# Optimization experiments

Hardware: AMD Instinct MI355X
Metric: run time of the kernel (lower is better)

## Reference

```python
import jax, jax.numpy as jnp
import numpy as np
from jax import lax

WIN = 5
WIN_SIZE = float(WIN * WIN * WIN)


def _box_sum(x):
    # 5x5x5 all-ones box-filter sum, stride 1, padding 2 (SAME), single channel.
    k = jnp.ones((1, 1, WIN, WIN, WIN), dtype=x.dtype)
    return lax.conv_general_dilated(
        x, k,
        window_strides=(1, 1, 1),
        padding=[(2, 2), (2, 2), (2, 2)],
        dimension_numbers=('NCDHW', 'OIDHW', 'NCDHW'))


def setup_inputs() -> dict:
    key = jax.random.key(0)
    k1, k2 = jax.random.split(key)
    shape = (2, 1, 160, 160, 160)
    real = jax.random.normal(k1, shape, dtype=jnp.float32)
    fake = jax.random.normal(k2, shape, dtype=jnp.float32)
    return {"real": real, "fake": fake}


def reference(real, fake):
    I2 = real * real
    J2 = fake * fake
    IJ = real * fake
    I_sum = _box_sum(real)
    J_sum = _box_sum(fake)
    I2_sum = _box_sum(I2)
    J2_sum = _box_sum(J2)
    IJ_sum = _box_sum(IJ)
    u_I = I_sum / WIN_SIZE
    u_J = J_sum / WIN_SIZE
    cross = IJ_sum - u_J * I_sum - u_I * J_sum + u_I * u_J * WIN_SIZE
    I_var = I2_sum - 2.0 * u_I * I_sum + u_I * u_I * WIN_SIZE
    J_var = J2_sum - 2.0 * u_J * J_sum + u_J * u_J * WIN_SIZE
    cc = cross * cross / (I_var * J_var + 1e-05)
    return jnp.mean(cc)
```

## Files before the change

kernel.cpp:

```cpp
#include <hip/hip_runtime.h>


#define DIM 160
#define SLAB (DIM * DIM)
#define VOL (DIM * DIM * DIM)
#define TD 8
#define ROWS 36
#define RST 44
#define NBLK 1000
#define NPART (NBLK * 4)

typedef float f4 __attribute__((ext_vector_type(4), aligned(16)));
typedef float f2 __attribute__((ext_vector_type(2), aligned(8)));

__device__ __forceinline__ f4 hwin(const f4 lo, const f4 hi) {
    const float c0 = ((lo.x + lo.y) + (lo.z + lo.w)) + hi.x;
    const float c1 = c0 - lo.x + hi.y;
    const float c2 = c1 - lo.y + hi.z;
    const float c3 = c2 - lo.z + hi.w;
    return (f4){c0, c1, c2, c3};
}

__global__ __launch_bounds__(256, 2) void ncc_main(const float* __restrict__ real,
                                                   const float* __restrict__ fake,
                                                   float* __restrict__ partials) {
    __shared__ __align__(16) float raw[2][2][ROWS][RST];

    const int tid = threadIdx.x;

    const int bid = blockIdx.x;
    const int vid = (bid & 7) * 125 + (bid >> 3);
    const int dz  = vid % 20;
    const int t1  = vid / 20;
    const int bx  = t1 % 5;
    const int by  = (t1 / 5) % 5;
    const int nb  = t1 / 25;
    const int w0 = 32 * bx, h0 = 32 * by, d0 = TD * dz;

    const float* baseI = real + (size_t)nb * VOL;
    const float* baseJ = fake + (size_t)nb * VOL;

    const int sr = tid >> 3;
    const int sc = tid & 7;
    const int co = sr * RST + 4 * sc;

    int gof[3], lof[3];
    bool ok[3], wlo[3];
    const float* src[3];
#pragma unroll
    for (int k = 0; k < 3; ++k) {
        const int t   = tid + 256 * k;
        const int tv  = t / 360;
        const int rem = t - 360 * tv;
        const int row = rem / 10;
        const int q   = rem - 10 * row;
        const int hg  = h0 - 2 + row;
        const int wq  = w0 - 4 + 4 * q;
        const bool okh = (unsigned)hg < DIM;
        const bool okw = (wq >= 0) && (wq + 3 < DIM);
        ok[k]  = (t < 720) && okh && okw;
        wlo[k] = ok[k] && (q > 0);
        gof[k] = hg * DIM + wq;
        lof[k] = (tv * ROWS + row) * RST + 4 * q - 2;
        src[k] = tv ? baseJ : baseI;
    }

    {
        float* L = &raw[0][0][0][0];
        for (int i = tid; i < 2 * 2 * ROWS * RST; i += 256) L[i] = 0.f;
    }
    __syncthreads();

    if (d0 > 0) {
        const size_t so = (size_t)(d0 - 2) * SLAB;
        float* L = &raw[0][0][0][0];
#pragma unroll
        for (int k = 0; k < 3; ++k) {
            if (ok[k]) {
                const f4 v = *(const f4*)(src[k] + so + gof[k]);
                if (wlo[k]) *(f2*)(L + lof[k]) = (f2){v.x, v.y};
                *(f2*)(L + lof[k] + 2) = (f2){v.z, v.w};
            }
        }
    }
    __syncthreads();

    const f4 zf = (f4){0.f, 0.f, 0.f, 0.f};
    f4 zs[5][5];
#pragma unroll
    for (int p = 0; p < 5; ++p)
#pragma unroll
        for (int q = 0; q < 5; ++q) zs[p][q] = zf;

    f4 acc = zf;
    const float inv = 1.0f / 125.0f;
    int cur = 0;

#pragma unroll 1
    for (int a = 0; a < 3; ++a) {
        const bool am0 = (a > 0);
#pragma unroll
        for (int b = 0; b < 5; ++b) {
            const bool compAct  = (a < 2) || (b < 2);
            const bool stageAct = (a < 2) || (b == 0);
            if (!compAct) continue;

            f4 v0 = zf, v1 = zf, v2 = zf;
            if (stageAct) {
                const int dd1 = d0 - 1 + 5 * a + b;
                if ((unsigned)dd1 < DIM) {
                    const size_t so = (size_t)dd1 * SLAB;
                    if (ok[0]) v0 = *(const f4*)(src[0] + so + gof[0]);
                    if (ok[1]) v1 = *(const f4*)(src[1] + so + gof[1]);
                    if (ok[2]) v2 = *(const f4*)(src[2] + so + gof[2]);
                }
            }

            const float* LI = &raw[cur][0][0][0];
            const float* LJ = &raw[cur][1][0][0];
            f4 vI0 = zf, vI1 = zf, vJ0 = zf, vJ1 = zf;
            f4 vI20 = zf, vI21 = zf, vJ20 = zf, vJ21 = zf, vIJ0 = zf, vIJ1 = zf;
#pragma unroll
            for (int t = 0; t < 5; ++t) {
                const int o = co + t * RST;
                const f4 a0 = *(const f4*)(LI + o);
                const f4 a1 = *(const f4*)(LI + o + 4);
                const f4 b0 = *(const f4*)(LJ + o);
                const f4 b1 = *(const f4*)(LJ + o + 4);
                vI0 += a0; vI1 += a1; vJ0 += b0; vJ1 += b1;
                vI20 += a0 * a0; vI21 += a1 * a1;
                vJ20 += b0 * b0; vJ21 += b1 * b1;
                vIJ0 += a0 * b0; vIJ1 += a1 * b1;
            }
            const f4 cs0 = hwin(vI0, vI1);
            const f4 cs1 = hwin(vJ0, vJ1);
            const f4 cs2 = hwin(vI20, vI21);
            const f4 cs3 = hwin(vJ20, vJ21);
            const f4 cs4 = hwin(vIJ0, vIJ1);

#pragma unroll
            for (int p = 0; p < 5; ++p) {
                const int kk  = (b - p + 5) % 5;
                const int bmk = b - kk;
                const bool doadd = (am0 || p <= b) &&
                                   (a == 0 || (a == 1 ? (bmk <= 2) : (bmk <= -3)));
                if (doadd) {
                    zs[p][0] += cs0; zs[p][1] += cs1; zs[p][2] += cs2;
                    zs[p][3] += cs3; zs[p][4] += cs4;
                }
            }

            const bool docomp = (a == 0) ? (b == 4) : ((a == 1) ? true : (b < 2));
            if (docomp) {
                const int pe = (b + 1) % 5;
                const f4 SI = zs[pe][0], SJ = zs[pe][1];
                const f4 S2I = zs[pe][2], S2J = zs[pe][3], SIJ = zs[pe][4];
                const f4 t0    = SI * inv;
                const f4 cross = SIJ - t0 * SJ;
                const f4 iv    = S2I - t0 * SI;
                const f4 jv    = S2J - (SJ * inv) * SJ;
                acc += cross * cross / (iv * jv + 1e-5f);
                zs[pe][0] = zf; zs[pe][1] = zf; zs[pe][2] = zf;
                zs[pe][3] = zf; zs[pe][4] = zf;
            }

            if (stageAct) {
                float* L = &raw[cur ^ 1][0][0][0];
                if (wlo[0]) *(f2*)(L + lof[0]) = (f2){v0.x, v0.y};
                if (ok[0])  *(f2*)(L + lof[0] + 2) = (f2){v0.z, v0.w};
                if (wlo[1]) *(f2*)(L + lof[1]) = (f2){v1.x, v1.y};
                if (ok[1])  *(f2*)(L + lof[1] + 2) = (f2){v1.z, v1.w};
                if (wlo[2]) *(f2*)(L + lof[2]) = (f2){v2.x, v2.y};
                if (ok[2])  *(f2*)(L + lof[2] + 2) = (f2){v2.z, v2.w};
            }
            __syncthreads();
            cur ^= 1;
        }
    }

    float a2 = (acc.x + acc.y) + (acc.z + acc.w);
#pragma unroll
    for (int off = 32; off; off >>= 1)
        a2 += __shfl_down(a2, off, 64);
    if ((tid & 63) == 0)
        partials[bid * 4 + (tid >> 6)] = a2;
}

__global__ void ncc_reduce(const float* __restrict__ partials, float* __restrict__ out) {
    __shared__ double ws[4];
    double s = 0.0;
    for (int i = threadIdx.x; i < NPART; i += 256) s += (double)partials[i];
#pragma unroll
    for (int off = 32; off; off >>= 1)
        s += __shfl_down(s, off, 64);
    if ((threadIdx.x & 63) == 0) ws[threadIdx.x >> 6] = s;
    __syncthreads();
    if (threadIdx.x == 0) {
        const double t = ws[0] + ws[1] + ws[2] + ws[3];
        out[0] = (float)(t / (2.0 * (double)VOL));
    }
}

extern "C" void kernel_launch(void* const* d_in, const int* in_sizes, int n_in,
                              void* d_out, int out_size, void* d_ws, size_t ws_size,
                              hipStream_t stream) {
    const float* real = (const float*)d_in[0];
    const float* fake = (const float*)d_in[1];
    float* out      = (float*)d_out;
    float* partials = (float*)d_ws;

    ncc_main<<<dim3(NBLK), dim3(256), 0, stream>>>(real, fake, partials);
    ncc_reduce<<<1, 256, 0, stream>>>(partials, out);
}
```

Baseline: 53.28 us.

## Halve tile height to 16 rows, two outputs per thread, doubling block count

```diff
diff --git a/kernel.cpp b/kernel.cpp
--- a/kernel.cpp
+++ b/kernel.cpp
@@ -5,21 +5,14 @@
 #define SLAB (DIM * DIM)
 #define VOL (DIM * DIM * DIM)
 #define TD 8
-#define ROWS 36
+#define TH 16
+#define ROWS 20
 #define RST 44
-#define NBLK 1000
+#define NBLK 2000
 #define NPART (NBLK * 4)
 
 typedef float f4 __attribute__((ext_vector_type(4), aligned(16)));
 typedef float f2 __attribute__((ext_vector_type(2), aligned(8)));
-
-__device__ __forceinline__ f4 hwin(const f4 lo, const f4 hi) {
-    const float c0 = ((lo.x + lo.y) + (lo.z + lo.w)) + hi.x;
-    const float c1 = c0 - lo.x + hi.y;
-    const float c2 = c1 - lo.y + hi.z;
-    const float c3 = c2 - lo.z + hi.w;
-    return (f4){c0, c1, c2, c3};
-}
 
 __global__ __launch_bounds__(256, 2) void ncc_main(const float* __restrict__ real,
                                                    const float* __restrict__ fake,
@@ -29,45 +22,42 @@
     const int tid = threadIdx.x;
 
     const int bid = blockIdx.x;
-    const int vid = (bid & 7) * 125 + (bid >> 3);
+    const int vid = (bid & 7) * 250 + (bid >> 3);
     const int dz  = vid % 20;
     const int t1  = vid / 20;
     const int bx  = t1 % 5;
-    const int by  = (t1 / 5) % 5;
-    const int nb  = t1 / 25;
-    const int w0 = 32 * bx, h0 = 32 * by, d0 = TD * dz;
+    const int by  = (t1 / 5) % 10;
+    const int nb  = t1 / 50;
+    const int w0 = 32 * bx, h0 = TH * by, d0 = TD * dz;
 
     const float* baseI = real + (size_t)nb * VOL;
     const float* baseJ = fake + (size_t)nb * VOL;
 
-    const int sr = tid >> 3;
-    const int sc = tid & 7;
-    const int co = sr * RST + 4 * sc;
-
-    int gof[3], lof[3];
-    bool ok[3], wlo[3];
-    const float* src[3];
-#pragma unroll
-    for (int k = 0; k < 3; ++k) {
+    const int sc = tid & 15;
+    const int sr = tid >> 4;
+    const int co = sr * RST + 2 * sc + 2;
+
+    int gof[2], lof[2];
+    bool ok[2];
+    const float* src[2];
+#pragma unroll
+    for (int k = 0; k < 2; ++k) {
         const int t   = tid + 256 * k;
-        const int tv  = t / 360;
-        const int rem = t - 360 * tv;
+        const int vv  = t / 200;
+        const int rem = t - 200 * vv;
         const int row = rem / 10;
         const int q   = rem - 10 * row;
         const int hg  = h0 - 2 + row;
         const int wq  = w0 - 4 + 4 * q;
-        const bool okh = (unsigned)hg < DIM;
-        const bool okw = (wq >= 0) && (wq + 3 < DIM);
-        ok[k]  = (t < 720) && okh && okw;
-        wlo[k] = ok[k] && (q > 0);
+        ok[k]  = (t < 400) && ((unsigned)hg < DIM) && (wq >= 0) && (wq + 3 < DIM);
         gof[k] = hg * DIM + wq;
-        lof[k] = (tv * ROWS + row) * RST + 4 * q - 2;
-        src[k] = tv ? baseJ : baseI;
+        lof[k] = (vv * ROWS + row) * RST + 4 * q;
+        src[k] = vv ? baseJ : baseI;
     }
 
     {
         float* L = &raw[0][0][0][0];
-        for (int i = tid; i < 2 * 2 * ROWS * RST; i += 256) L[i] = 0.f;
+        for (int i = tid; i < 880; i += 256) *(f4*)(L + 4 * i) = (f4){0.f, 0.f, 0.f, 0.f};
     }
     __syncthreads();
 
@@ -75,24 +65,20 @@
         const size_t so = (size_t)(d0 - 2) * SLAB;
         float* L = &raw[0][0][0][0];
 #pragma unroll
-        for (int k = 0; k < 3; ++k) {
-            if (ok[k]) {
-                const f4 v = *(const f4*)(src[k] + so + gof[k]);
-                if (wlo[k]) *(f2*)(L + lof[k]) = (f2){v.x, v.y};
-                *(f2*)(L + lof[k] + 2) = (f2){v.z, v.w};
-            }
-        }
+        for (int k = 0; k < 2; ++k)
+            if (ok[k]) *(f4*)(L + lof[k]) = *(const f4*)(src[k] + so + gof[k]);
     }
     __syncthreads();
 
+    const f2 z2 = (f2){0.f, 0.f};
     const f4 zf = (f4){0.f, 0.f, 0.f, 0.f};
-    f4 zs[5][5];
+    f2 zs[5][5];
 #pragma unroll
     for (int p = 0; p < 5; ++p)
 #pragma unroll
-        for (int q = 0; q < 5; ++q) zs[p][q] = zf;
-
-    f4 acc = zf;
+        for (int q = 0; q < 5; ++q) zs[p][q] = z2;
+
+    f2 acc = z2;
     const float inv = 1.0f / 125.0f;
     int cur = 0;
 
@@ -105,38 +91,43 @@
             const bool stageAct = (a < 2) || (b == 0);
             if (!compAct) continue;
 
-            f4 v0 = zf, v1 = zf, v2 = zf;
+            f4 v0 = zf, v1 = zf;
             if (stageAct) {
                 const int dd1 = d0 - 1 + 5 * a + b;
                 if ((unsigned)dd1 < DIM) {
                     const size_t so = (size_t)dd1 * SLAB;
                     if (ok[0]) v0 = *(const f4*)(src[0] + so + gof[0]);
                     if (ok[1]) v1 = *(const f4*)(src[1] + so + gof[1]);
-                    if (ok[2]) v2 = *(const f4*)(src[2] + so + gof[2]);
                 }
             }
 
-            const float* LI = &raw[cur][0][0][0];
-            const float* LJ = &raw[cur][1][0][0];
-            f4 vI0 = zf, vI1 = zf, vJ0 = zf, vJ1 = zf;
-            f4 vI20 = zf, vI21 = zf, vJ20 = zf, vJ21 = zf, vIJ0 = zf, vIJ1 = zf;
+            const float* LB = &raw[cur][0][0][0];
+            f2 A0 = z2, A1 = z2, A2v = z2, B0 = z2, B1 = z2, B2v = z2;
+            f2 A20 = z2, A21 = z2, A22 = z2, B20 = z2, B21 = z2, B22 = z2;
+            f2 P0 = z2, P1 = z2, P2 = z2;
 #pragma unroll
             for (int t = 0; t < 5; ++t) {
-                const int o = co + t * RST;
-                const f4 a0 = *(const f4*)(LI + o);
-                const f4 a1 = *(const f4*)(LI + o + 4);
-                const f4 b0 = *(const f4*)(LJ + o);
-                const f4 b1 = *(const f4*)(LJ + o + 4);
-                vI0 += a0; vI1 += a1; vJ0 += b0; vJ1 += b1;
-                vI20 += a0 * a0; vI21 += a1 * a1;
-                vJ20 += b0 * b0; vJ21 += b1 * b1;
-                vIJ0 += a0 * b0; vIJ1 += a1 * b1;
-            }
-            const f4 cs0 = hwin(vI0, vI1);
-            const f4 cs1 = hwin(vJ0, vJ1);
-            const f4 cs2 = hwin(vI20, vI21);
-            const f4 cs3 = hwin(vJ20, vJ21);
-            const f4 cs4 = hwin(vIJ0, vIJ1);
+                const float* rp = LB + co + t * RST;
+                const f2 a0 = *(const f2*)(rp);
+                const f2 a1 = *(const f2*)(rp + 2);
+                const f2 a2 = *(const f2*)(rp + 4);
+                const f2 b0 = *(const f2*)(rp + ROWS * RST);
+                const f2 b1 = *(const f2*)(rp + ROWS * RST + 2);
+                const f2 b2 = *(const f2*)(rp + ROWS * RST + 4);
+                A0 += a0; A1 += a1; A2v += a2;
+                B0 += b0; B1 += b1; B2v += b2;
+                A20 += a0 * a0; A21 += a1 * a1; A22 += a2 * a2;
+                B20 += b0 * b0; B21 += b1 * b1; B22 += b2 * b2;
+                P0 += a0 * b0; P1 += a1 * b1; P2 += a2 * b2;
+            }
+#define HW2(r0, r1, r2) ((f2){((r0.x + r0.y) + (r1.x + r1.y)) + r2.x, \
+                              ((r0.y + r1.x) + (r1.y + r2.x)) + r2.y})
+            const f2 cs0 = HW2(A0, A1, A2v);
+            const f2 cs1 = HW2(B0, B1, B2v);
+            const f2 cs2 = HW2(A20, A21, A22);
+            const f2 cs3 = HW2(B20, B21, B22);
+            const f2 cs4 = HW2(P0, P1, P2);
+#undef HW2
 
 #pragma unroll
             for (int p = 0; p < 5; ++p) {
@@ -153,32 +144,28 @@
             const bool docomp = (a == 0) ? (b == 4) : ((a == 1) ? true : (b < 2));
             if (docomp) {
                 const int pe = (b + 1) % 5;
-                const f4 SI = zs[pe][0], SJ = zs[pe][1];
-                const f4 S2I = zs[pe][2], S2J = zs[pe][3], SIJ = zs[pe][4];
-                const f4 t0    = SI * inv;
-                const f4 cross = SIJ - t0 * SJ;
-                const f4 iv    = S2I - t0 * SI;
-                const f4 jv    = S2J - (SJ * inv) * SJ;
+                const f2 SI = zs[pe][0], SJ = zs[pe][1];
+                const f2 S2I = zs[pe][2], S2J = zs[pe][3], SIJ = zs[pe][4];
+                const f2 t0    = SI * inv;
+                const f2 cross = SIJ - t0 * SJ;
+                const f2 iv    = S2I - t0 * SI;
+                const f2 jv    = S2J - (SJ * inv) * SJ;
                 acc += cross * cross / (iv * jv + 1e-5f);
-                zs[pe][0] = zf; zs[pe][1] = zf; zs[pe][2] = zf;
-                zs[pe][3] = zf; zs[pe][4] = zf;
+                zs[pe][0] = z2; zs[pe][1] = z2; zs[pe][2] = z2;
+                zs[pe][3] = z2; zs[pe][4] = z2;
             }
 
             if (stageAct) {
-                float* L = &raw[cur ^ 1][0][0][0];
-                if (wlo[0]) *(f2*)(L + lof[0]) = (f2){v0.x, v0.y};
-                if (ok[0])  *(f2*)(L + lof[0] + 2) = (f2){v0.z, v0.w};
-                if (wlo[1]) *(f2*)(L + lof[1]) = (f2){v1.x, v1.y};
-                if (ok[1])  *(f2*)(L + lof[1] + 2) = (f2){v1.z, v1.w};
-                if (wlo[2]) *(f2*)(L + lof[2]) = (f2){v2.x, v2.y};
-                if (ok[2])  *(f2*)(L + lof[2] + 2) = (f2){v2.z, v2.w};
+                float* LW = &raw[cur ^ 1][0][0][0];
+                if (ok[0]) *(f4*)(LW + lof[0]) = v0;
+                if (ok[1]) *(f4*)(LW + lof[1]) = v1;
             }
             __syncthreads();
             cur ^= 1;
         }
     }
 
-    float a2 = (acc.x + acc.y) + (acc.z + acc.w);
+    float a2 = acc.x + acc.y;
 #pragma unroll
     for (int off = 32; off; off >>= 1)
         a2 += __shfl_down(a2, off, 64);
```

New measurement: 58.15 us. 1.09x slower.
